# Kernel optimization log

Hardware: AMD Instinct MI355X
Metric: run time of the kernel (lower is better)

The kernel has to match this reference:

```python
import jax, jax.numpy as jnp
import numpy as np
from jax import lax

DIM = 128
DEPTH = 2
OUT_DIM = 256
DIM_HEAD = 64
HEADS = 8
WS = 16
INNER = DIM_HEAD * HEADS
EPS = 1e-5
SCALE = DIM_HEAD ** (-0.5)


def setup_inputs() -> dict:
    key = jax.random.key(0)
    ks = jax.random.split(key, 20)
    s = 0.02
    L = DEPTH
    inp = {
        "x": jax.random.normal(ks[0], (1, DIM, 256, 256), dtype=jnp.float32),
        "ln1_g": jnp.ones((L, DIM), dtype=jnp.float32),
        "ln1_b": jnp.zeros((L, DIM), dtype=jnp.float32),
        "wq": jax.random.normal(ks[1], (L, INNER, DIM), dtype=jnp.float32) * s,
        "wkv": jax.random.normal(ks[2], (L, 2 * INNER, DIM), dtype=jnp.float32) * s,
        "wo": jax.random.normal(ks[3], (L, DIM, INNER), dtype=jnp.float32) * s,
        "bo": jnp.zeros((L, DIM), dtype=jnp.float32),
        "ln2_g": jnp.ones((L, DIM), dtype=jnp.float32),
        "ln2_b": jnp.zeros((L, DIM), dtype=jnp.float32),
        "w_in": jax.random.normal(ks[4], (L, DIM, DIM), dtype=jnp.float32) * s,
        "b_in": jnp.zeros((L, DIM), dtype=jnp.float32),
        "w_c3": jax.random.normal(ks[5], (L, OUT_DIM, DIM, 3, 3), dtype=jnp.float32) * s,
        "b_c3": jnp.zeros((L, OUT_DIM), dtype=jnp.float32),
        "w_c1": jax.random.normal(ks[6], (L, DIM, OUT_DIM), dtype=jnp.float32) * s,
        "b_c1": jnp.zeros((L, DIM), dtype=jnp.float32),
        "w_outer": jax.random.normal(ks[7], (DIM, DIM), dtype=jnp.float32) * s,
        "b_outer": jnp.zeros((DIM,), dtype=jnp.float32),
    }
    return inp


def _layernorm(x, g, b):
    # channel-wise (dim=1) norm; note torch code uses (std + eps), not sqrt(var + eps)
    mean = jnp.mean(x, axis=1, keepdims=True)
    std = jnp.sqrt(jnp.var(x, axis=1, keepdims=True))
    return (x - mean) / (std + EPS) * g[None, :, None, None] + b[None, :, None, None]


def _conv1x1(w, x, b=None):
    y = jnp.einsum('oi,bihw->bohw', w, x)
    if b is not None:
        y = y + b[None, :, None, None]
    return y


def _to_windows(t, B, H, W):
    # [B, HEADS*DIM_HEAD, H, W] -> [B*HEADS*nx*ny, WS*WS, DIM_HEAD]
    nx, ny = H // WS, W // WS
    t = t.reshape(B, HEADS, DIM_HEAD, nx, WS, ny, WS)
    t = t.transpose(0, 1, 3, 5, 4, 6, 2)
    return t.reshape(B * HEADS * nx * ny, WS * WS, DIM_HEAD)


def _from_windows(t, B, H, W):
    nx, ny = H // WS, W // WS
    t = t.reshape(B, HEADS, nx, ny, WS, WS, DIM_HEAD)
    t = t.transpose(0, 1, 6, 2, 4, 3, 5)
    return t.reshape(B, HEADS * DIM_HEAD, H, W)


def _attention(x, wq_l, wkv_l, wo_l, bo_l):
    B, _, H, W = x.shape
    q = _conv1x1(wq_l, x)
    kv = _conv1x1(wkv_l, x)
    k, v = kv[:, :INNER], kv[:, INNER:]
    q = _to_windows(q, B, H, W)
    k = _to_windows(k, B, H, W)
    v = _to_windows(v, B, H, W)
    sim = jnp.einsum('bid,bjd->bij', q, k) * SCALE  # [nwin, 256, 256]
    attn = jax.nn.softmax(sim, axis=-1)
    out = jnp.einsum('bij,bjd->bid', attn, v)
    out = _from_windows(out, B, H, W)
    return _conv1x1(wo_l, out, bo_l)


def _feedforward(x, w_in_l, b_in_l, w_c3_l, b_c3_l, w_c1_l, b_c1_l):
    h = _conv1x1(w_in_l, x, b_in_l)
    h = lax.conv_general_dilated(h, w_c3_l, window_strides=(1, 1), padding='SAME',
                                 dimension_numbers=('NCHW', 'OIHW', 'NCHW'))
    h = h + b_c3_l[None, :, None, None]
    h = jax.nn.gelu(h, approximate=False)
    return _conv1x1(w_c1_l, h, b_c1_l)


def reference(x, ln1_g, ln1_b, wq, wkv, wo, bo, ln2_g, ln2_b,
              w_in, b_in, w_c3, b_c3, w_c1, b_c1, w_outer, b_outer):
    for l in range(DEPTH):
        xn = _layernorm(x, ln1_g[l], ln1_b[l])
        x = _attention(xn, wq[l], wkv[l], wo[l], bo[l]) + x
        xn = _layernorm(x, ln2_g[l], ln2_b[l])
        x = _feedforward(xn, w_in[l], b_in[l], w_c3[l], b_c3[l], w_c1[l], b_c1[l]) + x
    return _conv1x1(w_outer, x, b_outer) + x
```

## Files before the change

### kernel.cpp

```cpp
#include <hip/hip_runtime.h>
#include <hip/hip_bf16.h>
#include <math.h>

typedef __hip_bfloat16 bf16;
typedef float f4 __attribute__((ext_vector_type(4)));
typedef short s8 __attribute__((ext_vector_type(8)));
typedef unsigned int u2 __attribute__((ext_vector_type(2)));
typedef unsigned int u4v __attribute__((ext_vector_type(4)));

__device__ __forceinline__ void gload16(const void* g, char* l) {
  __builtin_amdgcn_global_load_lds(
      (const __attribute__((address_space(1))) unsigned int*)g,
      (__attribute__((address_space(3))) unsigned int*)l, 16, 0, 0);
}
__device__ __forceinline__ unsigned short bfr(float f) {
  bf16 h = __float2bfloat16(f);
  return *(unsigned short*)&h;
}
__device__ __forceinline__ unsigned int pk2(float a, float b) {
  return (unsigned int)bfr(a) | ((unsigned int)bfr(b) << 16);
}
__device__ __forceinline__ unsigned int pkt(float a, float b) {
  return __builtin_amdgcn_perm(__float_as_uint(b), __float_as_uint(a), 0x07060302u);
}

__global__ __launch_bounds__(256) void prep_w(
    const float* __restrict__ wq, const float* __restrict__ wkv,
    const float* __restrict__ wo, const float* __restrict__ win,
    const float* __restrict__ wc3, const float* __restrict__ wc1,
    const float* __restrict__ wout, ushort* __restrict__ cw)
{
  int i = blockIdx.x * 256 + threadIdx.x;
  float v;
  if (i < 131072) v = wq[i];
  else if (i < 393216) v = wkv[i - 131072];
  else if (i < 524288) v = wo[i - 393216];
  else if (i < 1146880) return;
  else if (i < 1212416) v = wc1[i - 1146880];
  else if (i < 1228800) v = wout[i - 1212416];
  else if (i < 1230848) { cw[i] = 0; return; }
  else return;
  cw[i] = bfr(v);
}

__global__ __launch_bounds__(128) void prep_fold(
    const float* __restrict__ wc3, const float* __restrict__ win,
    const float* __restrict__ b_in, ushort* __restrict__ cw3out,
    float* __restrict__ T)
{
  __shared__ float col[128][9];
  __shared__ float sred[2][9];
  const int lyr = blockIdx.x >> 8, m = blockIdx.x & 255;
  const int tid = threadIdx.x;
  const float* src = wc3 + (((size_t)lyr * 256 + m) * 128 + tid) * 9;
#pragma unroll
  for (int t = 0; t < 9; ++t) col[tid][t] = src[t];
  float bi = b_in[lyr * 128 + tid];
  float sb[9];
#pragma unroll
  for (int t = 0; t < 9; ++t) {
    float v = col[tid][t] * bi;
    v += __shfl_xor(v, 1, 64);  v += __shfl_xor(v, 2, 64);
    v += __shfl_xor(v, 4, 64);  v += __shfl_xor(v, 8, 64);
    v += __shfl_xor(v, 16, 64); v += __shfl_xor(v, 32, 64);
    sb[t] = v;
  }
  if ((tid & 63) == 0) {
#pragma unroll
    for (int t = 0; t < 9; ++t) sred[tid >> 6][t] = sb[t];
  }
  __syncthreads();
  float acc[9] = {0.f,0.f,0.f,0.f,0.f,0.f,0.f,0.f,0.f};
  const float* wrow = win + (size_t)lyr * 16384 + tid;
  for (int c = 0; c < 128; ++c) {
    float wv = wrow[(size_t)c * 128];
#pragma unroll
    for (int t = 0; t < 9; ++t) acc[t] += col[c][t] * wv;
  }
  ushort* dst = cw3out + (size_t)lyr * 294912 + (size_t)m * 1152 + tid;
#pragma unroll
  for (int t = 0; t < 9; ++t) dst[t * 128] = bfr(acc[t]);
  if (tid == 0) {
    float s[9];
#pragma unroll
    for (int t = 0; t < 9; ++t) s[t] = sred[0][t] + sred[1][t];
    float* Tl = T + lyr * 2304;
    Tl[0 * 256 + m] = s[0]+s[1]+s[2]+s[3]+s[4]+s[5]+s[6]+s[7]+s[8];
    Tl[1 * 256 + m] = s[0] + s[1] + s[2];
    Tl[2 * 256 + m] = s[6] + s[7] + s[8];
    Tl[3 * 256 + m] = s[0] + s[3] + s[6];
    Tl[4 * 256 + m] = s[2] + s[5] + s[8];
    Tl[5 * 256 + m] = s[0];
    Tl[6 * 256 + m] = s[2];
    Tl[7 * 256 + m] = s[6];
    Tl[8 * 256 + m] = s[8];
  }
}

template<bool NCHW>
__global__ __launch_bounds__(256) void ln_nhwc(
    const float* __restrict__ x, const float* __restrict__ g,
    const float* __restrict__ b, ushort* __restrict__ y)
{
  const int p = blockIdx.x * 256 + threadIdx.x;
  f4 v[32];
  float s = 0.f, s2 = 0.f;
  if constexpr (NCHW) {
#pragma unroll
    for (int i = 0; i < 32; ++i)
#pragma unroll
      for (int j = 0; j < 4; ++j) {
        float t = x[(size_t)(i * 4 + j) * 65536 + p];
        v[i][j] = t; s += t; s2 += t * t;
      }
  } else {
    const f4* base = (const f4*)(x + (size_t)p * 128);
#pragma unroll
    for (int i = 0; i < 32; ++i) {
      v[i] = base[i];
#pragma unroll
      for (int j = 0; j < 4; ++j) { s += v[i][j]; s2 += v[i][j] * v[i][j]; }
    }
  }
  float mean = s * (1.f / 128.f);
  float var = s2 * (1.f / 128.f) - mean * mean;
  var = var > 0.f ? var : 0.f;
  float inv = 1.f / (sqrtf(var) + 1e-5f);
  u2* dst = (u2*)(y + (size_t)p * 128);
#pragma unroll
  for (int i = 0; i < 32; ++i) {
    f4 gg = *(const f4*)(g + i * 4);
    f4 bb = *(const f4*)(b + i * 4);
    float f0 = (v[i][0] - mean) * inv * gg[0] + bb[0];
    float f1 = (v[i][1] - mean) * inv * gg[1] + bb[1];
    float f2 = (v[i][2] - mean) * inv * gg[2] + bb[2];
    float f3 = (v[i][3] - mean) * inv * gg[3] + bb[3];
    u2 st; st.x = pk2(f0, f1); st.y = pk2(f2, f3);
    dst[i] = st;
  }
}

template<int MODE>
__global__ __launch_bounds__(256) void gemm_nhwc(
    const ushort* __restrict__ A, const ushort* __restrict__ X,
    const float* __restrict__ bias, const float* __restrict__ res,
    void* __restrict__ out, ushort* __restrict__ out2,
    const ushort* __restrict__ A2,
    const float* __restrict__ lng, const float* __restrict__ lnb,
    ushort* __restrict__ xn, const int K, const int M)
{
  constexpr unsigned SMSZ = (MODE == 7) ? 65536u : 32768u;
  __shared__ __align__(16) char sm[SMSZ];
  const int tid = threadIdx.x, w = tid >> 6, l = tid & 63;
  const int quad = l >> 4, l15 = l & 15;
  const int n0 = blockIdx.x * 128, m0 = blockIdx.y * 128;
  const int mh = (w & 1) * 64, nh = (w >> 1) * 64;
  const f4 fz = {0.f, 0.f, 0.f, 0.f};
  f4 acc[4][4];
#pragma unroll
  for (int a = 0; a < 4; ++a)
#pragma unroll
    for (int b2 = 0; b2 < 4; ++b2) acc[a][b2] = fz;

  const int KI = K >> 6;
  for (int kk = 0; kk < KI; ++kk) {
    if (kk) __syncthreads();
    const int k0 = kk << 6;
#pragma unroll
    for (int j = 0; j < 4; ++j) {
      int p = j * 256 + tid, r = p >> 3, c = (p & 7) ^ (r & 7);
      gload16(A + (size_t)(m0 + r) * K + k0 + c * 8, sm + (j * 256 + w * 64) * 16);
    }
#pragma unroll
    for (int j = 0; j < 4; ++j) {
      int p = j * 256 + tid, r = p >> 3, c = (p & 7) ^ (r & 7);
      gload16(X + (size_t)(n0 + r) * K + k0 + c * 8, sm + 16384 + (j * 256 + w * 64) * 16);
    }
    __syncthreads();
#pragma unroll
    for (int ks = 0; ks < 2; ++ks) {
      s8 af[4], bx[4];
#pragma unroll
      for (int mt = 0; mt < 4; ++mt) {
        int rr = mh + mt * 16 + l15;
        af[mt] = *(const s8*)(sm + rr * 128 + (((ks * 4 + quad) ^ (rr & 7)) << 4));
      }
#pragma unroll
      for (int nt = 0; nt < 4; ++nt) {
        int rr = nh + nt * 16 + l15;
        bx[nt] = *(const s8*)(sm + 16384 + rr * 128 + (((ks * 4 + quad) ^ (rr & 7)) << 4));
      }
#pragma unroll
      for (int mt = 0; mt < 4; ++mt)
#pragma unroll
        for (int nt = 0; nt < 4; ++nt)
          acc[mt][nt] = __builtin_amdgcn_mfma_f32_16x16x32_bf16(af[mt], bx[nt], acc[mt][nt], 0, 0, 0);
    }
  }

  if constexpr (MODE == 7) {
#pragma unroll
    for (int mt = 0; mt < 4; ++mt) {
      const int m = mh + mt * 16 + quad * 4;
      f4 bb = *(const f4*)(bias + m);
      const int seg = m >> 6, kl = m & 63;
#pragma unroll
      for (int nt = 0; nt < 4; ++nt) {
        const int r = nh + nt * 16 + l15;
        f4 v = acc[mt][nt] + bb + *(const f4*)(res + (size_t)(n0 + r) * 128 + m);
        acc[mt][nt] = v;
        u2 st; st.x = pk2(v[0], v[1]); st.y = pk2(v[2], v[3]);
        *(u2*)(sm + 32768 + seg * 16384 + r * 128 +
               (((kl >> 3) ^ (r & 7)) << 4) + (kl & 7) * 2) = st;
      }
    }
    __syncthreads();
#pragma unroll
    for (int kk2 = 0; kk2 < 2; ++kk2)
#pragma unroll
      for (int j = 0; j < 4; ++j) {
        int p = j * 256 + tid, r = p >> 3, c = (p & 7) ^ (r & 7);
        gload16(A2 + (size_t)r * 128 + kk2 * 64 + c * 8,
                sm + kk2 * 16384 + (j * 256 + w * 64) * 16);
      }
    __syncthreads();
    f4 acc2[4][4];
#pragma unroll
    for (int a = 0; a < 4; ++a)
#pragma unroll
      for (int b2 = 0; b2 < 4; ++b2) acc2[a][b2] = fz;
#pragma unroll
    for (int kk2 = 0; kk2 < 2; ++kk2)
#pragma unroll
      for (int ks = 0; ks < 2; ++ks) {
        s8 af[4], bx[4];
#pragma unroll
        for (int mt = 0; mt < 4; ++mt) {
          int rr = mh + mt * 16 + l15;
          af[mt] = *(const s8*)(sm + kk2 * 16384 + rr * 128 + (((ks * 4 + quad) ^ (rr & 7)) << 4));
        }
#pragma unroll
        for (int nt = 0; nt < 4; ++nt) {
          int rr = nh + nt * 16 + l15;
          bx[nt] = *(const s8*)(sm + 32768 + kk2 * 16384 + rr * 128 + (((ks * 4 + quad) ^ (rr & 7)) << 4));
        }
#pragma unroll
        for (int mt = 0; mt < 4; ++mt)
#pragma unroll
          for (int nt = 0; nt < 4; ++nt)
            acc2[mt][nt] = __builtin_amdgcn_mfma_f32_16x16x32_bf16(af[mt], bx[nt], acc2[mt][nt], 0, 0, 0);
      }
#pragma unroll
    for (int mt = 0; mt < 4; ++mt) {
      const int m = mh + mt * 16 + quad * 4;
      f4 bo2 = *(const f4*)(lng + m);
#pragma unroll
      for (int nt = 0; nt < 4; ++nt) {
        const int n = n0 + nh + nt * 16 + l15;
        f4 v2 = acc2[mt][nt] + bo2 + acc[mt][nt];
#pragma unroll
        for (int i = 0; i < 4; ++i)
          ((float*)out)[(size_t)(m + i) * 65536 + n] = v2[i];
      }
    }
    return;
  }

  if constexpr (MODE == 5 || MODE == 6) {
    float s1[4] = {0.f, 0.f, 0.f, 0.f}, s2[4] = {0.f, 0.f, 0.f, 0.f};
#pragma unroll
    for (int mt = 0; mt < 4; ++mt) {
      const int m = mh + mt * 16 + quad * 4;
      f4 bb = *(const f4*)(bias + m);
#pragma unroll
      for (int nt = 0; nt < 4; ++nt) {
        const int n = n0 + nh + nt * 16 + l15;
        f4 v = acc[mt][nt] + bb;
        if constexpr (MODE == 5) {
          f4 r = *(const f4*)(res + (size_t)n * 128 + m);
          v += r;
        } else {
          f4 r;
#pragma unroll
          for (int i = 0; i < 4; ++i) r[i] = res[(size_t)(m + i) * 65536 + n];
          v += r;
        }
        *(f4*)((float*)out + (size_t)n * 128 + m) = v;
        acc[mt][nt] = v;
        s1[nt] += v[0] + v[1] + v[2] + v[3];
        s2[nt] += v[0] * v[0] + v[1] * v[1] + v[2] * v[2] + v[3] * v[3];
      }
    }
    __syncthreads();
    float* pb = (float*)sm;
#pragma unroll
    for (int nt = 0; nt < 4; ++nt) {
      float a1 = s1[nt], a2 = s2[nt];
      a1 += __shfl_xor(a1, 16, 64); a1 += __shfl_xor(a1, 32, 64);
      a2 += __shfl_xor(a2, 16, 64); a2 += __shfl_xor(a2, 32, 64);
      s1[nt] = a1; s2[nt] = a2;
      if (quad == 0) {
        int pn = nh + nt * 16 + l15;
        pb[((w & 1) * 128 + pn) * 2]     = a1;
        pb[((w & 1) * 128 + pn) * 2 + 1] = a2;
      }
    }
    __syncthreads();
#pragma unroll
    for (int nt = 0; nt < 4; ++nt) {
      int pn = nh + nt * 16 + l15;
      float t1 = s1[nt] + pb[((1 - (w & 1)) * 128 + pn) * 2];
      float t2 = s2[nt] + pb[((1 - (w & 1)) * 128 + pn) * 2 + 1];
      float mean = t1 * (1.f / 128.f);
      float var = t2 * (1.f / 128.f) - mean * mean;
      var = var > 0.f ? var : 0.f;
      s1[nt] = mean;
      s2[nt] = 1.f / (sqrtf(var) + 1e-5f);
    }
#pragma unroll
    for (int mt = 0; mt < 4; ++mt) {
      const int m = mh + mt * 16 + quad * 4;
      f4 gg = *(const f4*)(lng + m);
      f4 b2 = *(const f4*)(lnb + m);
#pragma unroll
      for (int nt = 0; nt < 4; ++nt) {
        const int n = n0 + nh + nt * 16 + l15;
        f4 v = acc[mt][nt];
        float mean = s1[nt], inv = s2[nt];
        float f0 = (v[0] - mean) * inv * gg[0] + b2[0];
        float f1 = (v[1] - mean) * inv * gg[1] + b2[1];
        float f2 = (v[2] - mean) * inv * gg[2] + b2[2];
        float f3 = (v[3] - mean) * inv * gg[3] + b2[3];
        u2 st; st.x = pk2(f0, f1); st.y = pk2(f2, f3);
        *(u2*)(xn + (size_t)n * 128 + m) = st;
      }
    }
    return;
  }

#pragma unroll
  for (int mt = 0; mt < 4; ++mt) {
#pragma unroll
    for (int nt = 0; nt < 4; ++nt) {
      const int m = m0 + mh + mt * 16 + quad * 4;
      const int n = n0 + nh + nt * 16 + l15;
      f4 bb = *(const f4*)(bias + m);
      f4 v = acc[mt][nt] + bb;
      if constexpr (MODE == 0) {
        u2 st; st.x = pk2(v[0], v[1]); st.y = pk2(v[2], v[3]);
        *(u2*)((ushort*)out + (size_t)n * M + m) = st;
      } else if constexpr (MODE == 1 || MODE == 3) {
        f4 r = *(const f4*)(res + (size_t)n * M + m);
        v += r;
        *(f4*)((float*)out + (size_t)n * M + m) = v;
        if constexpr (MODE == 3) {
          u2 st; st.x = pk2(v[0], v[1]); st.y = pk2(v[2], v[3]);
          *(u2*)(out2 + (size_t)n * M + m) = st;
        }
      } else if constexpr (MODE == 4) {
        f4 r;
#pragma unroll
        for (int i = 0; i < 4; ++i) r[i] = res[(size_t)(m + i) * 65536 + n];
        v += r;
        *(f4*)((float*)out + (size_t)n * M + m) = v;
      } else {
        f4 r = *(const f4*)(res + (size_t)n * M + m);
#pragma unroll
        for (int i = 0; i < 4; ++i)
          ((float*)out)[(size_t)(m + i) * 65536 + n] = v[i] + r[i];
      }
    }
  }
}

__global__ __launch_bounds__(256) void conv3_kernel(
    const ushort* __restrict__ A, const ushort* __restrict__ X,
    const float* __restrict__ bias, ushort* __restrict__ out,
    const ushort* __restrict__ zp, const float* __restrict__ T)
{
  __shared__ __align__(16) char sm[32768];
  const int tid = threadIdx.x, w = tid >> 6, l = tid & 63;
  const int quad = l >> 4, l15 = l & 15;
  const int n0 = blockIdx.x * 128, m0 = blockIdx.y * 128;
  const int mh = (w & 1) * 64, nh = (w >> 1) * 64;
  const f4 fz = {0.f, 0.f, 0.f, 0.f};
  f4 acc[4][4];
#pragma unroll
  for (int a = 0; a < 4; ++a)
#pragma unroll
    for (int b2 = 0; b2 < 4; ++b2) acc[a][b2] = fz;

  for (int kk = 0; kk < 18; ++kk) {
    if (kk) __syncthreads();
    const int tap = kk >> 1, ky = tap / 3, kx = tap - ky * 3;
    const int dn = (ky - 1) * 256 + (kx - 1);
    const int kseg = (kk & 1) << 6;
#pragma unroll
    for (int j = 0; j < 4; ++j) {
      int p = j * 256 + tid, r = p >> 3, c = (p & 7) ^ (r & 7);
      gload16(A + (size_t)(m0 + r) * 1152 + kk * 64 + c * 8, sm + (j * 256 + w * 64) * 16);
    }
#pragma unroll
    for (int j = 0; j < 4; ++j) {
      int p = j * 256 + tid, r = p >> 3, c = (p & 7) ^ (r & 7);
      int nl = n0 + r;
      int ys = (nl >> 8) + ky - 1, xs = (nl & 255) + kx - 1;
      const ushort* gp = ((unsigned)ys < 256u && (unsigned)xs < 256u)
                         ? X + (size_t)(nl + dn) * 128 + kseg + c * 8 : zp;
      gload16(gp, sm + 16384 + (j * 256 + w * 64) * 16);
    }
    __syncthreads();
#pragma unroll
    for (int ks = 0; ks < 2; ++ks) {
      s8 af[4], bx[4];
#pragma unroll
      for (int mt = 0; mt < 4; ++mt) {
        int rr = mh + mt * 16 + l15;
        af[mt] = *(const s8*)(sm + rr * 128 + (((ks * 4 + quad) ^ (rr & 7)) << 4));
      }
#pragma unroll
      for (int nt = 0; nt < 4; ++nt) {
        int rr = nh + nt * 16 + l15;
        bx[nt] = *(const s8*)(sm + 16384 + rr * 128 + (((ks * 4 + quad) ^ (rr & 7)) << 4));
      }
#pragma unroll
      for (int mt = 0; mt < 4; ++mt)
#pragma unroll
        for (int nt = 0; nt < 4; ++nt)
          acc[mt][nt] = __builtin_amdgcn_mfma_f32_16x16x32_bf16(af[mt], bx[nt], acc[mt][nt], 0, 0, 0);
    }
  }
  const int y = n0 >> 8;
  const bool y0 = (y == 0), y1 = (y == 255);
  const int xbase = (n0 & 255) + nh;
#pragma unroll
  for (int mt = 0; mt < 4; ++mt) {
    const int m = m0 + mh + mt * 16 + quad * 4;
    f4 base = *(const f4*)(bias + m) + *(const f4*)(T + m);
    f4 Lc = *(const f4*)(T + 3 * 256 + m);
    f4 Rc = *(const f4*)(T + 4 * 256 + m);
    if (y0) {
      base -= *(const f4*)(T + 1 * 256 + m);
      Lc -= *(const f4*)(T + 5 * 256 + m);
      Rc -= *(const f4*)(T + 6 * 256 + m);
    }
    if (y1) {
      base -= *(const f4*)(T + 2 * 256 + m);
      Lc -= *(const f4*)(T + 7 * 256 + m);
      Rc -= *(const f4*)(T + 8 * 256 + m);
    }
#pragma unroll
    for (int nt = 0; nt < 4; ++nt) {
      const int n = n0 + nh + nt * 16 + l15;
      const int x = xbase + nt * 16 + l15;
      float fx0 = (x == 0) ? 1.f : 0.f;
      float fx1 = (x == 255) ? 1.f : 0.f;
      f4 v = acc[mt][nt] + base - Lc * fx0 - Rc * fx1;
      float g0 = 0.5f * v[0] * (1.f + erff(v[0] * 0.70710678118f));
      float g1 = 0.5f * v[1] * (1.f + erff(v[1] * 0.70710678118f));
      float g2 = 0.5f * v[2] * (1.f + erff(v[2] * 0.70710678118f));
      float g3 = 0.5f * v[3] * (1.f + erff(v[3] * 0.70710678118f));
      u2 st; st.x = pk2(g0, g1); st.y = pk2(g2, g3);
      *(u2*)(out + (size_t)n * 256 + m) = st;
    }
  }
}

__global__ __launch_bounds__(512) void attn_kernel(
    const ushort* __restrict__ xn, const ushort* __restrict__ wq,
    const ushort* __restrict__ wkv, ushort* __restrict__ ao)
{
  __shared__ __align__(16) char sm[147456];
  const int tid = threadIdx.x, w = tid >> 6, l = tid & 63;
  const int quad = l >> 4, l15 = l & 15;
  const int win = blockIdx.x, head = blockIdx.y;
  const int nbase = ((win >> 4) << 12) + ((win & 15) << 4);
  char* RX  = sm;
  char* RW  = sm + 65536;
  char* RK  = sm + 114688;
  char* RVT = sm;
  char* Pw  = sm + 32768 + w * 4096;
  char* RO  = RW;
  const f4 fz = {0.f, 0.f, 0.f, 0.f};

#pragma unroll
  for (int j = 0; j < 8; ++j) {
    int p = j * 512 + tid, r = p >> 4, c = (p & 15) ^ (r & 15);
    int n = nbase + ((r >> 4) << 8) + (r & 15);
    gload16(xn + (size_t)n * 128 + c * 8, RX + (j * 512 + w * 64) * 16);
  }
  {
    const ushort* wpq = wq + (size_t)head * 64 * 128;
    const ushort* wpk = wkv + (size_t)head * 64 * 128;
    const ushort* wpv = wkv + (size_t)(512 + head * 64) * 128;
#pragma unroll
    for (int j = 0; j < 2; ++j) {
      int p = j * 512 + tid, r = p >> 4, c = (p & 15) ^ (r & 15);
      gload16(wpq + (size_t)r * 128 + c * 8, RW + (j * 512 + w * 64) * 16);
    }
#pragma unroll
    for (int j = 0; j < 2; ++j) {
      int p = j * 512 + tid, r = p >> 4, c = (p & 15) ^ (r & 15);
      gload16(wpk + (size_t)r * 128 + c * 8, RW + 16384 + (j * 512 + w * 64) * 16);
    }
#pragma unroll
    for (int j = 0; j < 2; ++j) {
      int p = j * 512 + tid, r = p >> 4, c = (p & 15) ^ (r & 15);
      gload16(wpv + (size_t)r * 128 + c * 8, RW + 32768 + (j * 512 + w * 64) * 16);
    }
  }
  __syncthreads();

  s8 bq[2][2];
  {
    f4 acc[4][2];
#pragma unroll
    for (int a = 0; a < 4; ++a) { acc[a][0] = fz; acc[a][1] = fz; }
#pragma unroll
    for (int ks = 0; ks < 4; ++ks) {
      s8 af[4], bx[2];
#pragma unroll
      for (int mt = 0; mt < 4; ++mt) {
        int rr = mt * 16 + l15;
        af[mt] = *(const s8*)(RW + rr * 256 + (((ks * 4 + quad) ^ (rr & 15)) << 4));
      }
#pragma unroll
      for (int nt = 0; nt < 2; ++nt) {
        int rr = w * 32 + nt * 16 + l15;
        bx[nt] = *(const s8*)(RX + rr * 256 + (((ks * 4 + quad) ^ (rr & 15)) << 4));
      }
#pragma unroll
      for (int mt = 0; mt < 4; ++mt)
#pragma unroll
        for (int nt = 0; nt < 2; ++nt)
          acc[mt][nt] = __builtin_amdgcn_mfma_f32_16x16x32_bf16(af[mt], bx[nt], acc[mt][nt], 0, 0, 0);
    }
#pragma unroll
    for (int nt = 0; nt < 2; ++nt) {
      unsigned pd[4][2];
#pragma unroll
      for (int mt = 0; mt < 4; ++mt) {
        pd[mt][0] = pkt(acc[mt][nt][0], acc[mt][nt][1]);
        pd[mt][1] = pkt(acc[mt][nt][2], acc[mt][nt][3]);
      }
#pragma unroll
      for (int ks = 0; ks < 2; ++ks) {
        u4v t;
#pragma unroll
        for (int dj = 0; dj < 4; ++dj) {
          int srcl = l15 + (((quad & 1) * 2 + (dj >> 1)) << 4);
          unsigned va = (unsigned)__shfl((int)pd[2 * ks][dj & 1], srcl, 64);
          unsigned vb = (unsigned)__shfl((int)pd[2 * ks + 1][dj & 1], srcl, 64);
          t[dj] = (quad < 2) ? va : vb;
        }
        bq[nt][ks] = __builtin_bit_cast(s8, t);
      }
    }
  }

  {
    f4 acc[4][2];
#pragma unroll
    for (int a = 0; a < 4; ++a) { acc[a][0] = fz; acc[a][1] = fz; }
#pragma unroll
    for (int ks = 0; ks < 4; ++ks) {
      s8 af[4], bx[2];
#pragma unroll
      for (int mt = 0; mt < 4; ++mt) {
        int rr = mt * 16 + l15;
        af[mt] = *(const s8*)(RW + 16384 + rr * 256 + (((ks * 4 + quad) ^ (rr & 15)) << 4));
      }
#pragma unroll
      for (int nt = 0; nt < 2; ++nt) {
        int rr = w * 32 + nt * 16 + l15;
        bx[nt] = *(const s8*)(RX + rr * 256 + (((ks * 4 + quad) ^ (rr & 15)) << 4));
      }
#pragma unroll
      for (int mt = 0; mt < 4; ++mt)
#pragma unroll
        for (int nt = 0; nt < 2; ++nt)
          acc[mt][nt] = __builtin_amdgcn_mfma_f32_16x16x32_bf16(af[mt], bx[nt], acc[mt][nt], 0, 0, 0);
    }
#pragma unroll
    for (int mt = 0; mt < 4; ++mt)
#pragma unroll
      for (int nt = 0; nt < 2; ++nt) {
        int tok = w * 32 + nt * 16 + l15, d0 = mt * 16 + quad * 4;
        char* a = RK + tok * 128 + (((d0 >> 3) ^ (tok & 7)) << 4) + (d0 & 7) * 2;
        *(unsigned int*)a = pkt(acc[mt][nt][0], acc[mt][nt][1]);
        *(unsigned int*)(a + 4) = pkt(acc[mt][nt][2], acc[mt][nt][3]);
      }
  }

  {
    f4 acc[2][4];
#pragma unroll
    for (int a = 0; a < 2; ++a)
#pragma unroll
      for (int b2 = 0; b2 < 4; ++b2) acc[a][b2] = fz;
#pragma unroll
    for (int ks = 0; ks < 4; ++ks) {
      s8 ax[2], bw[4];
#pragma unroll
      for (int mt = 0; mt < 2; ++mt) {
        int rr = w * 32 + mt * 16 + l15;
        ax[mt] = *(const s8*)(RX + rr * 256 + (((ks * 4 + quad) ^ (rr & 15)) << 4));
      }
#pragma unroll
      for (int nt = 0; nt < 4; ++nt) {
        int rr = nt * 16 + l15;
        bw[nt] = *(const s8*)(RW + 32768 + rr * 256 + (((ks * 4 + quad) ^ (rr & 15)) << 4));
      }
#pragma unroll
      for (int mt = 0; mt < 2; ++mt)
#pragma unroll
        for (int nt = 0; nt < 4; ++nt)
          acc[mt][nt] = __builtin_amdgcn_mfma_f32_16x16x32_bf16(ax[mt], bw[nt], acc[mt][nt], 0, 0, 0);
    }
    __syncthreads();
#pragma unroll
    for (int mt = 0; mt < 2; ++mt)
#pragma unroll
      for (int nt = 0; nt < 4; ++nt) {
        int d = nt * 16 + l15, t0 = w * 32 + mt * 16 + quad * 4;
        char* a = RVT + d * 512 + (((t0 >> 3) ^ (d & 31)) << 4) + (t0 & 7) * 2;
        *(unsigned int*)a = pkt(acc[mt][nt][0], acc[mt][nt][1]);
        *(unsigned int*)(a + 4) = pkt(acc[mt][nt][2], acc[mt][nt][3]);
      }
  }
  __syncthreads();

  f4 o[4][2];
  float lsum[2] = {0.f, 0.f};
#pragma unroll
  for (int a = 0; a < 4; ++a) { o[a][0] = fz; o[a][1] = fz; }

  for (int jt = 0; jt < 4; ++jt) {
    f4 s[4][2];
#pragma unroll
    for (int a = 0; a < 4; ++a) { s[a][0] = fz; s[a][1] = fz; }
#pragma unroll
    for (int ks = 0; ks < 2; ++ks) {
      s8 af[4];
#pragma unroll
      for (int mt = 0; mt < 4; ++mt) {
        int rr = jt * 64 + mt * 16 + l15;
        af[mt] = *(const s8*)(RK + rr * 128 + (((ks * 4 + quad) ^ (rr & 7)) << 4));
      }
      __builtin_amdgcn_s_setprio(1);
#pragma unroll
      for (int mt = 0; mt < 4; ++mt)
#pragma unroll
        for (int nt = 0; nt < 2; ++nt)
          s[mt][nt] = __builtin_amdgcn_mfma_f32_16x16x32_bf16(af[mt], bq[nt][ks], s[mt][nt], 0, 0, 0);
      __builtin_amdgcn_s_setprio(0);
    }
#pragma unroll
    for (int mt = 0; mt < 4; ++mt)
#pragma unroll
      for (int nt = 0; nt < 2; ++nt) {
        float p0 = exp2f(s[mt][nt][0] * 0.18033688f);
        float p1 = exp2f(s[mt][nt][1] * 0.18033688f);
        float p2 = exp2f(s[mt][nt][2] * 0.18033688f);
        float p3 = exp2f(s[mt][nt][3] * 0.18033688f);
        lsum[nt] += p0 + p1 + p2 + p3;
        int iL = nt * 16 + l15, j0 = mt * 16 + quad * 4;
        char* a = Pw + iL * 128 + (((j0 >> 3) ^ (iL & 7)) << 4) + (j0 & 7) * 2;
        *(unsigned int*)a = pkt(p0, p1);
        *(unsigned int*)(a + 4) = pkt(p2, p3);
      }
#pragma unroll
    for (int ks = 0; ks < 2; ++ks) {
      s8 av[4], bp[2];
#pragma unroll
      for (int mt = 0; mt < 4; ++mt) {
        int d = mt * 16 + l15;
        av[mt] = *(const s8*)(RVT + d * 512 + (((jt * 8 + ks * 4 + quad) ^ (d & 31)) << 4));
      }
#pragma unroll
      for (int nt = 0; nt < 2; ++nt) {
        int iL = nt * 16 + l15;
        bp[nt] = *(const s8*)(Pw + iL * 128 + (((ks * 4 + quad) ^ (iL & 7)) << 4));
      }
      __builtin_amdgcn_s_setprio(1);
#pragma unroll
      for (int mt = 0; mt < 4; ++mt)
#pragma unroll
        for (int nt = 0; nt < 2; ++nt)
          o[mt][nt] = __builtin_amdgcn_mfma_f32_16x16x32_bf16(av[mt], bp[nt], o[mt][nt], 0, 0, 0);
      __builtin_amdgcn_s_setprio(0);
    }
  }

  float inv[2];
#pragma unroll
  for (int nt = 0; nt < 2; ++nt) {
    float v = lsum[nt];
    v += __shfl_xor(v, 16, 64);
    v += __shfl_xor(v, 32, 64);
    inv[nt] = 1.f / v;
  }
#pragma unroll
  for (int mt = 0; mt < 4; ++mt)
#pragma unroll
    for (int nt = 0; nt < 2; ++nt) {
      int i = w * 32 + nt * 16 + l15, d0 = mt * 16 + quad * 4;
      char* a = RO + i * 128 + (((d0 >> 3) ^ (i & 7)) << 4) + (d0 & 7) * 2;
      *(unsigned int*)a = pkt(o[mt][nt][0] * inv[nt], o[mt][nt][1] * inv[nt]);
      *(unsigned int*)(a + 4) = pkt(o[mt][nt][2] * inv[nt], o[mt][nt][3] * inv[nt]);
    }
  __syncthreads();
  const int tok = tid >> 1, half = tid & 1;
  const int n = nbase + ((tok >> 4) << 8) + (tok & 15);
  ushort* dst = ao + (size_t)n * 512 + head * 64 + half * 32;
#pragma unroll
  for (int c = 0; c < 4; ++c) {
    u4v v = *(const u4v*)(RO + tok * 128 + (((half * 4 + c) ^ (tok & 7)) << 4));
    *(u4v*)(dst + c * 8) = v;
  }
}

extern "C" void kernel_launch(void* const* d_in, const int* in_sizes, int n_in,
                              void* d_out, int out_size, void* d_ws, size_t ws_size,
                              hipStream_t stream)
{
  const float* x_in    = (const float*)d_in[0];
  const float* ln1_g   = (const float*)d_in[1];
  const float* ln1_b   = (const float*)d_in[2];
  const float* wq      = (const float*)d_in[3];
  const float* wkv     = (const float*)d_in[4];
  const float* wo      = (const float*)d_in[5];
  const float* bo      = (const float*)d_in[6];
  const float* ln2_g   = (const float*)d_in[7];
  const float* ln2_b   = (const float*)d_in[8];
  const float* w_in    = (const float*)d_in[9];
  const float* b_in    = (const float*)d_in[10];
  const float* w_c3    = (const float*)d_in[11];
  const float* b_c3    = (const float*)d_in[12];
  const float* w_c1    = (const float*)d_in[13];
  const float* b_c1    = (const float*)d_in[14];
  const float* w_outer = (const float*)d_in[15];
  const float* b_outer = (const float*)d_in[16];

  char* wsb = (char*)d_ws;
  ushort* CW = (ushort*)wsb;
  float*  TB = (float*)(wsb + 3145728);
  float*  XH = (float*)(wsb + 4194304);
  ushort* XN = (ushort*)(wsb + 37748736);
  ushort* AO = (ushort*)(wsb + 54525952);
  ushort* G  = (ushort*)(wsb + 138412032);

  const ushort* zp = CW + 1228800;
  dim3 b256(256);

  prep_w<<<dim3(4808), b256, 0, stream>>>(wq, wkv, wo, w_in, w_c3, w_c1, w_outer, CW);
  prep_fold<<<dim3(512), dim3(128), 0, stream>>>(w_c3, w_in, b_in, CW + 557056, TB);

  ln_nhwc<true><<<dim3(256), b256, 0, stream>>>(x_in, ln1_g, ln1_b, XN);
  attn_kernel<<<dim3(256, 8), dim3(512), 0, stream>>>(XN, CW, CW + 131072, AO);
  gemm_nhwc<6><<<dim3(512, 1), b256, 0, stream>>>(CW + 393216, AO, bo, x_in, XH,
      nullptr, nullptr, ln2_g, ln2_b, XN, 512, 128);
  conv3_kernel<<<dim3(512, 2), b256, 0, stream>>>(CW + 557056, XN, b_c3, G, zp, TB);
  gemm_nhwc<5><<<dim3(512, 1), b256, 0, stream>>>(CW + 1146880, G, b_c1, XH, XH,
      nullptr, nullptr, ln1_g + 128, ln1_b + 128, XN, 256, 128);

  attn_kernel<<<dim3(256, 8), dim3(512), 0, stream>>>(XN, CW + 65536, CW + 262144, AO);
  gemm_nhwc<5><<<dim3(512, 1), b256, 0, stream>>>(CW + 458752, AO, bo + 128, XH, XH,
      nullptr, nullptr, ln2_g + 128, ln2_b + 128, XN, 512, 128);
  conv3_kernel<<<dim3(512, 2), b256, 0, stream>>>(CW + 851968, XN, b_c3 + 256, G, zp, TB + 2304);
  gemm_nhwc<7><<<dim3(512, 1), b256, 0, stream>>>(CW + 1179648, G, b_c1 + 128, XH, d_out,
      nullptr, CW + 1212416, b_outer, nullptr, nullptr, 256, 128);
}
```

Baseline: 576.4 us.

## Double attention block to 1024 threads with 16 query rows per wave

The window-attention kernel now runs 16 waves per block instead of 8. Each wave owns 16 query tokens instead of 32, so the per-wave tiles for the Q/K/V projections, scores and output all shrink and the P scratch per wave is halved. The intent is more latency hiding and less register pressure per wave, since LDS use (144KB) already limits each CU to one block. The cost is that every wave now reloads the same shared K/V/weight fragments for half as much MFMA work, which raises LDS read traffic relative to compute.

```diff
diff --git a/kernel.cpp b/kernel.cpp
--- a/kernel.cpp
+++ b/kernel.cpp
@@ -466,7 +466,7 @@
   }
 }
 
-__global__ __launch_bounds__(512) void attn_kernel(
+__global__ __launch_bounds__(1024) void attn_kernel(
     const ushort* __restrict__ xn, const ushort* __restrict__ wq,
     const ushort* __restrict__ wkv, ushort* __restrict__ ao)
 {
@@ -479,166 +479,129 @@
   char* RW  = sm + 65536;
   char* RK  = sm + 114688;
   char* RVT = sm;
-  char* Pw  = sm + 32768 + w * 4096;
+  char* Pw  = sm + 32768 + w * 2048;
   char* RO  = RW;
   const f4 fz = {0.f, 0.f, 0.f, 0.f};
-
-#pragma unroll
-  for (int j = 0; j < 8; ++j) {
-    int p = j * 512 + tid, r = p >> 4, c = (p & 15) ^ (r & 15);
+  const int tokw = w * 16 + l15;
+
+#pragma unroll
+  for (int j = 0; j < 4; ++j) {
+    int p = j * 1024 + tid, r = p >> 4, c = (p & 15) ^ (r & 15);
     int n = nbase + ((r >> 4) << 8) + (r & 15);
-    gload16(xn + (size_t)n * 128 + c * 8, RX + (j * 512 + w * 64) * 16);
+    gload16(xn + (size_t)n * 128 + c * 8, RX + (j * 1024 + w * 64) * 16);
   }
   {
     const ushort* wpq = wq + (size_t)head * 64 * 128;
     const ushort* wpk = wkv + (size_t)head * 64 * 128;
     const ushort* wpv = wkv + (size_t)(512 + head * 64) * 128;
-#pragma unroll
-    for (int j = 0; j < 2; ++j) {
-      int p = j * 512 + tid, r = p >> 4, c = (p & 15) ^ (r & 15);
-      gload16(wpq + (size_t)r * 128 + c * 8, RW + (j * 512 + w * 64) * 16);
-    }
-#pragma unroll
-    for (int j = 0; j < 2; ++j) {
-      int p = j * 512 + tid, r = p >> 4, c = (p & 15) ^ (r & 15);
-      gload16(wpk + (size_t)r * 128 + c * 8, RW + 16384 + (j * 512 + w * 64) * 16);
-    }
-#pragma unroll
-    for (int j = 0; j < 2; ++j) {
-      int p = j * 512 + tid, r = p >> 4, c = (p & 15) ^ (r & 15);
-      gload16(wpv + (size_t)r * 128 + c * 8, RW + 32768 + (j * 512 + w * 64) * 16);
-    }
+    int r = tid >> 4, c = (tid & 15) ^ (r & 15);
+    gload16(wpq + (size_t)r * 128 + c * 8, RW + w * 1024);
+    gload16(wpk + (size_t)r * 128 + c * 8, RW + 16384 + w * 1024);
+    gload16(wpv + (size_t)r * 128 + c * 8, RW + 32768 + w * 1024);
   }
   __syncthreads();
 
-  s8 bq[2][2];
+  s8 bq[2];
   {
-    f4 acc[4][2];
-#pragma unroll
-    for (int a = 0; a < 4; ++a) { acc[a][0] = fz; acc[a][1] = fz; }
+    f4 acc[4];
+#pragma unroll
+    for (int a = 0; a < 4; ++a) acc[a] = fz;
 #pragma unroll
     for (int ks = 0; ks < 4; ++ks) {
-      s8 af[4], bx[2];
+      s8 af[4], bx;
 #pragma unroll
       for (int mt = 0; mt < 4; ++mt) {
         int rr = mt * 16 + l15;
         af[mt] = *(const s8*)(RW + rr * 256 + (((ks * 4 + quad) ^ (rr & 15)) << 4));
       }
-#pragma unroll
-      for (int nt = 0; nt < 2; ++nt) {
-        int rr = w * 32 + nt * 16 + l15;
-        bx[nt] = *(const s8*)(RX + rr * 256 + (((ks * 4 + quad) ^ (rr & 15)) << 4));
-      }
+      bx = *(const s8*)(RX + tokw * 256 + (((ks * 4 + quad) ^ (tokw & 15)) << 4));
 #pragma unroll
       for (int mt = 0; mt < 4; ++mt)
-#pragma unroll
-        for (int nt = 0; nt < 2; ++nt)
-          acc[mt][nt] = __builtin_amdgcn_mfma_f32_16x16x32_bf16(af[mt], bx[nt], acc[mt][nt], 0, 0, 0);
-    }
-#pragma unroll
-    for (int nt = 0; nt < 2; ++nt) {
-      unsigned pd[4][2];
-#pragma unroll
-      for (int mt = 0; mt < 4; ++mt) {
-        pd[mt][0] = pkt(acc[mt][nt][0], acc[mt][nt][1]);
-        pd[mt][1] = pkt(acc[mt][nt][2], acc[mt][nt][3]);
-      }
-#pragma unroll
-      for (int ks = 0; ks < 2; ++ks) {
-        u4v t;
-#pragma unroll
-        for (int dj = 0; dj < 4; ++dj) {
-          int srcl = l15 + (((quad & 1) * 2 + (dj >> 1)) << 4);
-          unsigned va = (unsigned)__shfl((int)pd[2 * ks][dj & 1], srcl, 64);
-          unsigned vb = (unsigned)__shfl((int)pd[2 * ks + 1][dj & 1], srcl, 64);
-          t[dj] = (quad < 2) ? va : vb;
-        }
-        bq[nt][ks] = __builtin_bit_cast(s8, t);
-      }
+        acc[mt] = __builtin_amdgcn_mfma_f32_16x16x32_bf16(af[mt], bx, acc[mt], 0, 0, 0);
+    }
+    unsigned pd[4][2];
+#pragma unroll
+    for (int mt = 0; mt < 4; ++mt) {
+      pd[mt][0] = pkt(acc[mt][0], acc[mt][1]);
+      pd[mt][1] = pkt(acc[mt][2], acc[mt][3]);
+    }
+#pragma unroll
+    for (int ks = 0; ks < 2; ++ks) {
+      u4v t;
+#pragma unroll
+      for (int dj = 0; dj < 4; ++dj) {
+        int srcl = l15 + (((quad & 1) * 2 + (dj >> 1)) << 4);
+        unsigned va = (unsigned)__shfl((int)pd[2 * ks][dj & 1], srcl, 64);
+        unsigned vb = (unsigned)__shfl((int)pd[2 * ks + 1][dj & 1], srcl, 64);
+        t[dj] = (quad < 2) ? va : vb;
+      }
+      bq[ks] = __builtin_bit_cast(s8, t);
     }
   }
 
   {
-    f4 acc[4][2];
-#pragma unroll
-    for (int a = 0; a < 4; ++a) { acc[a][0] = fz; acc[a][1] = fz; }
+    f4 acc[4];
+#pragma unroll
+    for (int a = 0; a < 4; ++a) acc[a] = fz;
 #pragma unroll
     for (int ks = 0; ks < 4; ++ks) {
-      s8 af[4], bx[2];
+      s8 af[4], bx;
 #pragma unroll
       for (int mt = 0; mt < 4; ++mt) {
         int rr = mt * 16 + l15;
         af[mt] = *(const s8*)(RW + 16384 + rr * 256 + (((ks * 4 + quad) ^ (rr & 15)) << 4));
       }
-#pragma unroll
-      for (int nt = 0; nt < 2; ++nt) {
-        int rr = w * 32 + nt * 16 + l15;
-        bx[nt] = *(const s8*)(RX + rr * 256 + (((ks * 4 + quad) ^ (rr & 15)) << 4));
-      }
+      bx = *(const s8*)(RX + tokw * 256 + (((ks * 4 + quad) ^ (tokw & 15)) << 4));
 #pragma unroll
       for (int mt = 0; mt < 4; ++mt)
-#pragma unroll
-        for (int nt = 0; nt < 2; ++nt)
-          acc[mt][nt] = __builtin_amdgcn_mfma_f32_16x16x32_bf16(af[mt], bx[nt], acc[mt][nt], 0, 0, 0);
-    }
-#pragma unroll
-    for (int mt = 0; mt < 4; ++mt)
-#pragma unroll
-      for (int nt = 0; nt < 2; ++nt) {
-        int tok = w * 32 + nt * 16 + l15, d0 = mt * 16 + quad * 4;
-        char* a = RK + tok * 128 + (((d0 >> 3) ^ (tok & 7)) << 4) + (d0 & 7) * 2;
-        *(unsigned int*)a = pkt(acc[mt][nt][0], acc[mt][nt][1]);
-        *(unsigned int*)(a + 4) = pkt(acc[mt][nt][2], acc[mt][nt][3]);
-      }
+        acc[mt] = __builtin_amdgcn_mfma_f32_16x16x32_bf16(af[mt], bx, acc[mt], 0, 0, 0);
+    }
+#pragma unroll
+    for (int mt = 0; mt < 4; ++mt) {
+      int d0 = mt * 16 + quad * 4;
+      char* a = RK + tokw * 128 + (((d0 >> 3) ^ (tokw & 7)) << 4) + (d0 & 7) * 2;
+      *(unsigned int*)a = pkt(acc[mt][0], acc[mt][1]);
+      *(unsigned int*)(a + 4) = pkt(acc[mt][2], acc[mt][3]);
+    }
   }
 
   {
-    f4 acc[2][4];
-#pragma unroll
-    for (int a = 0; a < 2; ++a)
-#pragma unroll
-      for (int b2 = 0; b2 < 4; ++b2) acc[a][b2] = fz;
+    f4 acc[4];
+#pragma unroll
+    for (int a = 0; a < 4; ++a) acc[a] = fz;
 #pragma unroll
     for (int ks = 0; ks < 4; ++ks) {
-      s8 ax[2], bw[4];
-#pragma unroll
-      for (int mt = 0; mt < 2; ++mt) {
-        int rr = w * 32 + mt * 16 + l15;
-        ax[mt] = *(const s8*)(RX + rr * 256 + (((ks * 4 + quad) ^ (rr & 15)) << 4));
-      }
+      s8 ax, bw[4];
+      ax = *(const s8*)(RX + tokw * 256 + (((ks * 4 + quad) ^ (tokw & 15)) << 4));
 #pragma unroll
       for (int nt = 0; nt < 4; ++nt) {
         int rr = nt * 16 + l15;
         bw[nt] = *(const s8*)(RW + 32768 + rr * 256 + (((ks * 4 + quad) ^ (rr & 15)) << 4));
       }
 #pragma unroll
-      for (int mt = 0; mt < 2; ++mt)
-#pragma unroll
-        for (int nt = 0; nt < 4; ++nt)
-          acc[mt][nt] = __builtin_amdgcn_mfma_f32_16x16x32_bf16(ax[mt], bw[nt], acc[mt][nt], 0, 0, 0);
+      for (int nt = 0; nt < 4; ++nt)
+        acc[nt] = __builtin_amdgcn_mfma_f32_16x16x32_bf16(ax, bw[nt], acc[nt], 0, 0, 0);
     }
     __syncthreads();
 #pragma unroll
-    for (int mt = 0; mt < 2; ++mt)
-#pragma unroll
-      for (int nt = 0; nt < 4; ++nt) {
-        int d = nt * 16 + l15, t0 = w * 32 + mt * 16 + quad * 4;
-        char* a = RVT + d * 512 + (((t0 >> 3) ^ (d & 31)) << 4) + (t0 & 7) * 2;
-        *(unsigned int*)a = pkt(acc[mt][nt][0], acc[mt][nt][1]);
-        *(unsigned int*)(a + 4) = pkt(acc[mt][nt][2], acc[mt][nt][3]);
-      }
+    for (int nt = 0; nt < 4; ++nt) {
+      int d = nt * 16 + l15, t0 = w * 16 + quad * 4;
+      char* a = RVT + d * 512 + (((t0 >> 3) ^ (d & 31)) << 4) + (t0 & 7) * 2;
+      *(unsigned int*)a = pkt(acc[nt][0], acc[nt][1]);
+      *(unsigned int*)(a + 4) = pkt(acc[nt][2], acc[nt][3]);
+    }
   }
   __syncthreads();
 
-  f4 o[4][2];
-  float lsum[2] = {0.f, 0.f};
-#pragma unroll
-  for (int a = 0; a < 4; ++a) { o[a][0] = fz; o[a][1] = fz; }
+  f4 o[4];
+  float lsum = 0.f;
+#pragma unroll
+  for (int a = 0; a < 4; ++a) o[a] = fz;
 
   for (int jt = 0; jt < 4; ++jt) {
-    f4 s[4][2];
-#pragma unroll
-    for (int a = 0; a < 4; ++a) { s[a][0] = fz; s[a][1] = fz; }
+    f4 s[4];
+#pragma unroll
+    for (int a = 0; a < 4; ++a) s[a] = fz;
 #pragma unroll
     for (int ks = 0; ks < 2; ++ks) {
       s8 af[4];
@@ -650,73 +613,58 @@
       __builtin_amdgcn_s_setprio(1);
 #pragma unroll
       for (int mt = 0; mt < 4; ++mt)
-#pragma unroll
-        for (int nt = 0; nt < 2; ++nt)
-          s[mt][nt] = __builtin_amdgcn_mfma_f32_16x16x32_bf16(af[mt], bq[nt][ks], s[mt][nt], 0, 0, 0);
+        s[mt] = __builtin_amdgcn_mfma_f32_16x16x32_bf16(af[mt], bq[ks], s[mt], 0, 0, 0);
       __builtin_amdgcn_s_setprio(0);
     }
 #pragma unroll
-    for (int mt = 0; mt < 4; ++mt)
-#pragma unroll
-      for (int nt = 0; nt < 2; ++nt) {
-        float p0 = exp2f(s[mt][nt][0] * 0.18033688f);
-        float p1 = exp2f(s[mt][nt][1] * 0.18033688f);
-        float p2 = exp2f(s[mt][nt][2] * 0.18033688f);
-        float p3 = exp2f(s[mt][nt][3] * 0.18033688f);
-        lsum[nt] += p0 + p1 + p2 + p3;
-        int iL = nt * 16 + l15, j0 = mt * 16 + quad * 4;
-        char* a = Pw + iL * 128 + (((j0 >> 3) ^ (iL & 7)) << 4) + (j0 & 7) * 2;
-        *(unsigned int*)a = pkt(p0, p1);
-        *(unsigned int*)(a + 4) = pkt(p2, p3);
-      }
+    for (int mt = 0; mt < 4; ++mt) {
+      float p0 = exp2f(s[mt][0] * 0.18033688f);
+      float p1 = exp2f(s[mt][1] * 0.18033688f);
+      float p2 = exp2f(s[mt][2] * 0.18033688f);
+      float p3 = exp2f(s[mt][3] * 0.18033688f);
+      lsum += p0 + p1 + p2 + p3;
+      int j0 = mt * 16 + quad * 4;
+      char* a = Pw + l15 * 128 + (((j0 >> 3) ^ (l15 & 7)) << 4) + (j0 & 7) * 2;
+      *(unsigned int*)a = pkt(p0, p1);
+      *(unsigned int*)(a + 4) = pkt(p2, p3);
+    }
 #pragma unroll
     for (int ks = 0; ks < 2; ++ks) {
-      s8 av[4], bp[2];
+      s8 av[4], bp;
 #pragma unroll
       for (int mt = 0; mt < 4; ++mt) {
         int d = mt * 16 + l15;
         av[mt] = *(const s8*)(RVT + d * 512 + (((jt * 8 + ks * 4 + quad) ^ (d & 31)) << 4));
       }
-#pragma unroll
-      for (int nt = 0; nt < 2; ++nt) {
-        int iL = nt * 16 + l15;
-        bp[nt] = *(const s8*)(Pw + iL * 128 + (((ks * 4 + quad) ^ (iL & 7)) << 4));
-      }
+      bp = *(const s8*)(Pw + l15 * 128 + (((ks * 4 + quad) ^ (l15 & 7)) << 4));
       __builtin_amdgcn_s_setprio(1);
 #pragma unroll
       for (int mt = 0; mt < 4; ++mt)
-#pragma unroll
-        for (int nt = 0; nt < 2; ++nt)
-          o[mt][nt] = __builtin_amdgcn_mfma_f32_16x16x32_bf16(av[mt], bp[nt], o[mt][nt], 0, 0, 0);
+        o[mt] = __builtin_amdgcn_mfma_f32_16x16x32_bf16(av[mt], bp, o[mt], 0, 0, 0);
       __builtin_amdgcn_s_setprio(0);
     }
   }
 
-  float inv[2];
-#pragma unroll
-  for (int nt = 0; nt < 2; ++nt) {
-    float v = lsum[nt];
-    v += __shfl_xor(v, 16, 64);
-    v += __shfl_xor(v, 32, 64);
-    inv[nt] = 1.f / v;
-  }
-#pragma unroll
-  for (int mt = 0; mt < 4; ++mt)
-#pragma unroll
-    for (int nt = 0; nt < 2; ++nt) {
-      int i = w * 32 + nt * 16 + l15, d0 = mt * 16 + quad * 4;
-      char* a = RO + i * 128 + (((d0 >> 3) ^ (i & 7)) << 4) + (d0 & 7) * 2;
-      *(unsigned int*)a = pkt(o[mt][nt][0] * inv[nt], o[mt][nt][1] * inv[nt]);
-      *(unsigned int*)(a + 4) = pkt(o[mt][nt][2] * inv[nt], o[mt][nt][3] * inv[nt]);
-    }
+  float lv = lsum;
+  lv += __shfl_xor(lv, 16, 64);
+  lv += __shfl_xor(lv, 32, 64);
+  const float inv = 1.f / lv;
+#pragma unroll
+  for (int mt = 0; mt < 4; ++mt) {
+    int i = w * 16 + l15, d0 = mt * 16 + quad * 4;
+    char* a = RO + i * 128 + (((d0 >> 3) ^ (i & 7)) << 4) + (d0 & 7) * 2;
+    *(unsigned int*)a = pkt(o[mt][0] * inv, o[mt][1] * inv);
+    *(unsigned int*)(a + 4) = pkt(o[mt][2] * inv, o[mt][3] * inv);
+  }
   __syncthreads();
-  const int tok = tid >> 1, half = tid & 1;
+  const int tok = tid >> 2, q2 = tid & 3;
   const int n = nbase + ((tok >> 4) << 8) + (tok & 15);
-  ushort* dst = ao + (size_t)n * 512 + head * 64 + half * 32;
-#pragma unroll
-  for (int c = 0; c < 4; ++c) {
-    u4v v = *(const u4v*)(RO + tok * 128 + (((half * 4 + c) ^ (tok & 7)) << 4));
-    *(u4v*)(dst + c * 8) = v;
+  ushort* dst = ao + (size_t)n * 512 + head * 64;
+#pragma unroll
+  for (int c = 0; c < 2; ++c) {
+    int chunk = q2 * 2 + c;
+    u4v v = *(const u4v*)(RO + tok * 128 + ((chunk ^ (tok & 7)) << 4));
+    *(u4v*)(dst + chunk * 8) = v;
   }
 }
 
@@ -757,14 +705,14 @@
   prep_fold<<<dim3(512), dim3(128), 0, stream>>>(w_c3, w_in, b_in, CW + 557056, TB);
 
   ln_nhwc<true><<<dim3(256), b256, 0, stream>>>(x_in, ln1_g, ln1_b, XN);
-  attn_kernel<<<dim3(256, 8), dim3(512), 0, stream>>>(XN, CW, CW + 131072, AO);
+  attn_kernel<<<dim3(256, 8), dim3(1024), 0, stream>>>(XN, CW, CW + 131072, AO);
   gemm_nhwc<6><<<dim3(512, 1), b256, 0, stream>>>(CW + 393216, AO, bo, x_in, XH,
       nullptr, nullptr, ln2_g, ln2_b, XN, 512, 128);
   conv3_kernel<<<dim3(512, 2), b256, 0, stream>>>(CW + 557056, XN, b_c3, G, zp, TB);
   gemm_nhwc<5><<<dim3(512, 1), b256, 0, stream>>>(CW + 1146880, G, b_c1, XH, XH,
       nullptr, nullptr, ln1_g + 128, ln1_b + 128, XN, 256, 128);
 
-  attn_kernel<<<dim3(256, 8), dim3(512), 0, stream>>>(XN, CW + 65536, CW + 262144, AO);
+  attn_kernel<<<dim3(256, 8), dim3(1024), 0, stream>>>(XN, CW + 65536, CW + 262144, AO);
   gemm_nhwc<5><<<dim3(512, 1), b256, 0, stream>>>(CW + 458752, AO, bo + 128, XH, XH,
       nullptr, nullptr, ln2_g + 128, ln2_b + 128, XN, 512, 128);
   conv3_kernel<<<dim3(512, 2), b256, 0, stream>>>(CW + 851968, XN, b_c3 + 256, G, zp, TB + 2304);
```

Result: slower. 648.4 us (+12.5%).
